# Performance work log

Hardware: AMD Instinct MI355X
Metric: run time of the kernel (lower is better)

Reference implementation:

```python
import jax, jax.numpy as jnp
import numpy as np

MIN_TIMESCALE = 1.0
MAX_TIMESCALE = 10000.0


def llama_rope(x):
    # x: [B, S, N, H]; LLaMA-style interleaved rotary embedding (pairs along last dim).
    B, S, N, H = x.shape
    half = H // 2
    fraction = 2.0 * jnp.arange(0, half, dtype=jnp.float32) / H
    timescale = MIN_TIMESCALE * (MAX_TIMESCALE / MIN_TIMESCALE) ** fraction  # [half]
    position = jnp.arange(S, dtype=jnp.float32)[None, :, None, None]  # [1,S,1,1]
    sinusoid = position / timescale[None, None, None, :]  # [1,S,1,half]
    sin, cos = jnp.sin(sinusoid), jnp.cos(sinusoid)
    xr = x.astype(jnp.float32).reshape(B, S, N, half, 2)
    x1, x2 = xr[..., 0], xr[..., 1]
    r1 = x1 * cos - x2 * sin
    r2 = x2 * cos + x1 * sin
    out = jnp.stack((r1, r2), axis=-1).reshape(B, S, N, H)
    return out.astype(x.dtype)


def setup_inputs() -> dict:
    key = jax.random.key(0)
    kx, kq, kk, kv, ko = jax.random.split(key, 5)
    B, S, D, N, H = 4, 2048, 2048, 16, 128
    x = jax.random.normal(kx, (B, S, D), dtype=jnp.float32)
    # fan_in-style scaling for projection kernels
    wq = jax.random.normal(kq, (D, N, H), dtype=jnp.float32) / np.sqrt(D)
    wk = jax.random.normal(kk, (D, N, H), dtype=jnp.float32) / np.sqrt(D)
    wv = jax.random.normal(kv, (D, N, H), dtype=jnp.float32) / np.sqrt(D)
    wo = jax.random.normal(ko, (N, H, D), dtype=jnp.float32) / np.sqrt(N * H)
    return {"x": x, "wq": wq, "wk": wk, "wv": wv, "wo": wo}


def reference(x, wq, wk, wv, wo):
    # QKV projections (DenseGeneral with features=(num_heads, head_dim))
    q = jnp.einsum("bsd,dnh->bsnh", x, wq)
    k = jnp.einsum("bsd,dnh->bsnh", x, wk)
    v = jnp.einsum("bsd,dnh->bsnh", x, wv)
    # Fused RoPE on query and key (LLaMA interleaved variant)
    q = llama_rope(q)
    k = llama_rope(k)
    head_dim = q.shape[-1]
    q = q / jnp.sqrt(jnp.asarray(head_dim, q.dtype))
    # Causal flash attention (math equivalent: masked softmax attention)
    S = q.shape[1]
    logits = jnp.einsum("bqnh,bknh->bnqk", q, k)  # [B,N,S,S]
    causal = jnp.tril(jnp.ones((S, S), dtype=bool))
    logits = jnp.where(causal[None, None, :, :], logits, jnp.asarray(-1e30, logits.dtype))
    probs = jax.nn.softmax(logits.astype(jnp.float32), axis=-1).astype(v.dtype)
    attn = jnp.einsum("bnqk,bknh->bqnh", probs, v)  # [B,S,N,H]
    # Output projection (DenseGeneral over axes (-2,-1))
    return jnp.einsum("bqnh,nhd->bqd", attn, wo)
```

## Files before the change

kernel.cpp:

```cpp
#include <hip/hip_runtime.h>
#include <hip/hip_bf16.h>
#include <cmath>

#define S_LEN 2048
#define DDIM  2048
#define NHEAD 16
#define HDIM  128
#define BATCH 4
#define KPAD  152
#define VPAD  40
#define PPAD  40

typedef __bf16 bf16;
typedef __attribute__((ext_vector_type(8))) __bf16 bf16x8;
typedef __attribute__((ext_vector_type(4))) __bf16 bf16x4;
typedef __attribute__((ext_vector_type(4))) float  f32x4;

__device__ __forceinline__ void gl_lds(const bf16* g, bf16* l) {
  __builtin_amdgcn_global_load_lds((const __attribute__((address_space(1))) unsigned*)g,
                                   (__attribute__((address_space(3))) unsigned*)l, 16, 0, 0);
}

__global__ __launch_bounds__(256)
void conv_kernel(const float* __restrict__ x, bf16* __restrict__ y) {
  size_t i = ((size_t)blockIdx.x * 256 + threadIdx.x) * 8;
  float4 a = *(const float4*)&x[i];
  float4 b = *(const float4*)&x[i + 4];
  bf16x8 o;
  o[0] = (bf16)a.x; o[1] = (bf16)a.y; o[2] = (bf16)a.z; o[3] = (bf16)a.w;
  o[4] = (bf16)b.x; o[5] = (bf16)b.y; o[6] = (bf16)b.z; o[7] = (bf16)b.w;
  *(bf16x8*)&y[i] = o;
}

__global__ __launch_bounds__(256)
void twconv_kernel(const float* __restrict__ W, bf16* __restrict__ Wt) {
  __shared__ bf16 tile[64][72];
  const int t  = threadIdx.x;
  const int k0 = blockIdx.x * 64;
  const int n0 = blockIdx.y * 64;
#pragma unroll
  for (int it = 0; it < 4; it++) {
    int k = (t >> 4) + it * 16;
    int n = (t & 15) * 4;
    float4 v = *(const float4*)&W[(size_t)(k0 + k) * DDIM + n0 + n];
    tile[k][n + 0] = (bf16)v.x; tile[k][n + 1] = (bf16)v.y;
    tile[k][n + 2] = (bf16)v.z; tile[k][n + 3] = (bf16)v.w;
  }
  __syncthreads();
#pragma unroll
  for (int it = 0; it < 2; it++) {
    int n  = (t >> 3) + it * 32;
    int kc = (t & 7) * 8;
    bf16x8 o;
#pragma unroll
    for (int j = 0; j < 8; j++) o[j] = tile[kc + j][n];
    *(bf16x8*)&Wt[(size_t)(n0 + n) * DDIM + k0 + kc] = o;
  }
}

template <int MODE>
__global__ __launch_bounds__(512, 2)
void gemm_kernel(const bf16* __restrict__ A, const bf16* __restrict__ Bt,
                 void* __restrict__ Out) {
  __shared__ bf16 As[2][256 * 64];
  __shared__ bf16 Bs[2][256 * 64];

  const int t    = threadIdx.x;
  const int m0   = blockIdx.y * 256;
  const int n0   = blockIdx.x * 256;
  const int lane = t & 63;
  const int wave = t >> 6;
  const int wm   = wave >> 2;
  const int wn   = wave & 3;
  const int quad = lane >> 4;
  const int lm   = lane & 15;
  const int sw   = lm & 7;

  const int lrow   = lane >> 3;
  const int lslot  = lane & 7;
  const int lchunk = lslot ^ lrow;

  const int rA = wm * 128 + wn * 32;
  const int rB = (wn >> 1) * 128 + (wm * 2 + (wn & 1)) * 32;
  const bf16* gA = &A [(size_t)(m0 + rA + lrow) * DDIM + lchunk * 8];
  const bf16* gB = &Bt[(size_t)(n0 + rB + lrow) * DDIM + lchunk * 8];

  f32x4 acc[8][4];
#pragma unroll
  for (int i = 0; i < 8; i++)
#pragma unroll
    for (int j = 0; j < 4; j++) acc[i][j] = (f32x4){0.f, 0.f, 0.f, 0.f};

  auto stage = [&](int k0, int b) {
#pragma unroll
    for (int q = 0; q < 4; q++) {
      gl_lds(gA + (size_t)q * 8 * DDIM + k0, &As[b][(rA + q * 8) * 64]);
      gl_lds(gB + (size_t)q * 8 * DDIM + k0, &Bs[b][(rB + q * 8) * 64]);
    }
  };

  stage(0, 0);
  stage(64, 1);
  asm volatile("s_waitcnt vmcnt(8)" ::: "memory");
  __builtin_amdgcn_s_barrier();

  const int NT = DDIM / 64;
#pragma unroll 2
  for (int tt = 0; tt < NT; ++tt) {
    const bf16* as = &As[tt & 1][0];
    const bf16* bs = &Bs[tt & 1][0];
    bf16x8 af[4], bfr[4];

#pragma unroll
    for (int j = 0; j < 4; j++)
      bfr[j] = *(const bf16x8*)&bs[(wn * 64 + j * 16 + lm) * 64 + 8 * (quad ^ sw)];
#pragma unroll
    for (int i = 0; i < 4; i++)
      af[i] = *(const bf16x8*)&as[(wm * 128 + i * 16 + lm) * 64 + 8 * (quad ^ sw)];
    __builtin_amdgcn_s_setprio(1);
#pragma unroll
    for (int i = 0; i < 4; i++)
#pragma unroll
      for (int j = 0; j < 4; j++)
        acc[i][j] = __builtin_amdgcn_mfma_f32_16x16x32_bf16(af[i], bfr[j], acc[i][j], 0, 0, 0);
    __builtin_amdgcn_s_setprio(0);
    __builtin_amdgcn_sched_barrier(0);

#pragma unroll
    for (int i = 0; i < 4; i++)
      af[i] = *(const bf16x8*)&as[(wm * 128 + 64 + i * 16 + lm) * 64 + 8 * (quad ^ sw)];
    __builtin_amdgcn_s_setprio(1);
#pragma unroll
    for (int i = 0; i < 4; i++)
#pragma unroll
      for (int j = 0; j < 4; j++)
        acc[4 + i][j] = __builtin_amdgcn_mfma_f32_16x16x32_bf16(af[i], bfr[j], acc[4 + i][j], 0, 0, 0);
    __builtin_amdgcn_s_setprio(0);
    __builtin_amdgcn_sched_barrier(0);

#pragma unroll
    for (int j = 0; j < 4; j++)
      bfr[j] = *(const bf16x8*)&bs[(wn * 64 + j * 16 + lm) * 64 + 8 * ((4 + quad) ^ sw)];
#pragma unroll
    for (int i = 0; i < 4; i++)
      af[i] = *(const bf16x8*)&as[(wm * 128 + i * 16 + lm) * 64 + 8 * ((4 + quad) ^ sw)];
    __builtin_amdgcn_s_setprio(1);
#pragma unroll
    for (int i = 0; i < 4; i++)
#pragma unroll
      for (int j = 0; j < 4; j++)
        acc[i][j] = __builtin_amdgcn_mfma_f32_16x16x32_bf16(af[i], bfr[j], acc[i][j], 0, 0, 0);
    __builtin_amdgcn_s_setprio(0);
    __builtin_amdgcn_sched_barrier(0);

#pragma unroll
    for (int i = 0; i < 4; i++)
      af[i] = *(const bf16x8*)&as[(wm * 128 + 64 + i * 16 + lm) * 64 + 8 * ((4 + quad) ^ sw)];
    __builtin_amdgcn_s_setprio(1);
#pragma unroll
    for (int i = 0; i < 4; i++)
#pragma unroll
      for (int j = 0; j < 4; j++)
        acc[4 + i][j] = __builtin_amdgcn_mfma_f32_16x16x32_bf16(af[i], bfr[j], acc[4 + i][j], 0, 0, 0);
    __builtin_amdgcn_s_setprio(0);
    __builtin_amdgcn_sched_barrier(0);

    asm volatile("s_waitcnt lgkmcnt(0)" ::: "memory");
    __builtin_amdgcn_s_barrier();
    if (tt + 2 < NT) {
      stage((tt + 2) * 64, tt & 1);
      asm volatile("s_waitcnt vmcnt(8)" ::: "memory");
      __builtin_amdgcn_s_barrier();
    } else if (tt + 1 < NT) {
      asm volatile("s_waitcnt vmcnt(0)" ::: "memory");
      __builtin_amdgcn_s_barrier();
    }
  }

  const int row_base = m0 + wm * 128;
  const int col_base = n0 + wn * 64;

  if constexpr (MODE == 3) {
    float* O = (float*)Out;
#pragma unroll
    for (int m = 0; m < 8; m++)
#pragma unroll
      for (int j = 0; j < 4; j++)
#pragma unroll
        for (int r = 0; r < 4; r++) {
          int row = row_base + (m >> 2) * 64 + (m & 3) * 16 + quad * 4 + r;
          int col = col_base + j * 16 + lm;
          O[(size_t)row * DDIM + col] = acc[m][j][r];
        }
  } else if constexpr (MODE == 2) {
    bf16* O = (bf16*)Out;
#pragma unroll
    for (int m = 0; m < 8; m++) {
      int row = row_base + (m >> 2) * 64 + (m & 3) * 16 + quad * 4;
      int b = row >> 11, s = row & (S_LEN - 1);
#pragma unroll
      for (int j = 0; j < 4; j++) {
        int col = col_base + j * 16 + lm;
        int head = col >> 7, h = col & (HDIM - 1);
        bf16x4 pk;
#pragma unroll
        for (int r = 0; r < 4; r++) pk[r] = (bf16)acc[m][j][r];
        *(bf16x4*)&O[((size_t)(b * NHEAD + head) * HDIM + h) * S_LEN + s] = pk;
      }
    }
  } else {
    bf16* O = (bf16*)Out;
#pragma unroll
    for (int m = 0; m < 8; m++)
#pragma unroll
      for (int j = 0; j < 4; j++)
#pragma unroll
        for (int r = 0; r < 4; r++) {
          int row = row_base + (m >> 2) * 64 + (m & 3) * 16 + quad * 4 + r;
          int col = col_base + j * 16 + lm;
          int b = row >> 11, s = row & (S_LEN - 1);
          int head = col >> 7, h = col & (HDIM - 1);
          float v = acc[m][j][r];
          float partner = __shfl_xor(v, 1, 64);
          float inv_ts = __expf((float)(h >> 1) * -0.14391156831f);
          float ang = (float)s * inv_ts;
          float sn, cs;
          __sincosf(ang, &sn, &cs);
          float o = ((h & 1) == 0) ? (v * cs - partner * sn) : (v * cs + partner * sn);
          if (MODE == 0) o *= 0.08838834764831845f;
          O[((size_t)(b * NHEAD + head) * S_LEN + s) * HDIM + h] = (bf16)o;
        }
  }
}

__global__ __launch_bounds__(256, 2)
void attn_kernel(const bf16* __restrict__ Q, const bf16* __restrict__ K,
                 const bf16* __restrict__ Vt, bf16* __restrict__ Aout) {
  __shared__ bf16 Ks[32 * KPAD];
  __shared__ bf16 Vs[128 * VPAD];
  __shared__ bf16 Pl[4][32 * PPAD];
  const int t    = threadIdx.x;
  const int lane = t & 63;
  const int wave = t >> 6;
  const int quad = lane >> 4;
  const int lm   = lane & 15;
  const int a    = blockIdx.x;
  const int bh   = blockIdx.y;
  const int lobase = a * 64 + wave * 16;
  const int hibase = 2048 - a * 64 - 64 + wave * 16;
  const size_t hb = (size_t)bh * S_LEN * HDIM;
  const bf16* Qh = Q + hb;
  const bf16* Kh = K + hb;
  const bf16* Vh = Vt + hb;
  bf16* P = &Pl[wave][0];

  bf16x8 qflo[4], qfhi[4];
#pragma unroll
  for (int c = 0; c < 4; c++) {
    qflo[c] = *(const bf16x8*)&Qh[(size_t)(lobase + lm) * HDIM + c * 32 + quad * 8];
    qfhi[c] = *(const bf16x8*)&Qh[(size_t)(hibase + lm) * HDIM + c * 32 + quad * 8];
  }

  bf16 onev = (bf16)1.0f;
  bf16x8 ones = {onev, onev, onev, onev, onev, onev, onev, onev};

  f32x4 olo[8], ohi[8];
#pragma unroll
  for (int hc = 0; hc < 8; hc++) {
    olo[hc] = (f32x4){0.f, 0.f, 0.f, 0.f};
    ohi[hc] = (f32x4){0.f, 0.f, 0.f, 0.f};
  }
  f32x4 llo = (f32x4){0.f, 0.f, 0.f, 0.f};
  f32x4 lhi = (f32x4){0.f, 0.f, 0.f, 0.f};

  const int nkt = 64 - 2 * a;
  const int nlo = 2 * a + (wave >> 1) + 1;
  const int nhi = 63 - 2 * a + (wave >> 1);

  const int c0    = t * 2;
  const int krow0 = c0 >> 4, kcol0 = (c0 & 15) * 8;
  const int vrow0 = c0 >> 2, vcol0 = (c0 & 3) * 8;

  for (int kt = 0; kt < nkt; kt++) {
    const int kb = kt * 32;
    __syncthreads();
    {
      const bf16* kg = &Kh[(size_t)(kb + krow0) * HDIM + kcol0];
      *(bf16x8*)&Ks[krow0 * KPAD + kcol0]     = *(const bf16x8*)kg;
      *(bf16x8*)&Ks[krow0 * KPAD + kcol0 + 8] = *(const bf16x8*)(kg + 8);
      const bf16* vg = &Vh[(size_t)vrow0 * S_LEN + kb + vcol0];
      *(bf16x8*)&Vs[vrow0 * VPAD + vcol0]     = *(const bf16x8*)vg;
      *(bf16x8*)&Vs[vrow0 * VPAD + vcol0 + 8] = *(const bf16x8*)(vg + 8);
    }
    __syncthreads();

    const bool hi_act = kt < nhi;
    const bool lo_act = kt < nlo;

    bf16x8 af[2][4];
#pragma unroll
    for (int cb = 0; cb < 2; cb++)
#pragma unroll
      for (int c = 0; c < 4; c++)
        af[cb][c] = *(const bf16x8*)&Ks[(cb * 16 + lm) * KPAD + c * 32 + quad * 8];

    if (hi_act) {
      f32x4 s[2] = {(f32x4){0.f, 0.f, 0.f, 0.f}, (f32x4){0.f, 0.f, 0.f, 0.f}};
#pragma unroll
      for (int c = 0; c < 4; c++)
#pragma unroll
        for (int cb = 0; cb < 2; cb++)
          s[cb] = __builtin_amdgcn_mfma_f32_16x16x32_bf16(af[cb][c], qfhi[c], s[cb], 0, 0, 0);
#pragma unroll
      for (int cb = 0; cb < 2; cb++) {
        bf16x4 pk;
#pragma unroll
        for (int r = 0; r < 4; r++) {
          int key = kb + cb * 16 + quad * 4 + r;
          float sv = (key <= hibase + lm) ? s[cb][r] : -3.0e38f;
          pk[r] = (bf16)__expf(sv - 12.0f);
        }
        *(bf16x4*)&P[(16 + lm) * PPAD + cb * 16 + quad * 4] = pk;
      }
    }
    if (lo_act) {
      f32x4 s[2] = {(f32x4){0.f, 0.f, 0.f, 0.f}, (f32x4){0.f, 0.f, 0.f, 0.f}};
#pragma unroll
      for (int c = 0; c < 4; c++)
#pragma unroll
        for (int cb = 0; cb < 2; cb++)
          s[cb] = __builtin_amdgcn_mfma_f32_16x16x32_bf16(af[cb][c], qflo[c], s[cb], 0, 0, 0);
#pragma unroll
      for (int cb = 0; cb < 2; cb++) {
        bf16x4 pk;
#pragma unroll
        for (int r = 0; r < 4; r++) {
          int key = kb + cb * 16 + quad * 4 + r;
          float sv = (key <= lobase + lm) ? s[cb][r] : -3.0e38f;
          pk[r] = (bf16)__expf(sv - 12.0f);
        }
        *(bf16x4*)&P[lm * PPAD + cb * 16 + quad * 4] = pk;
      }
    }
    __builtin_amdgcn_s_waitcnt(0xC07F);

    bf16x8 vf[8];
#pragma unroll
    for (int hc = 0; hc < 8; hc++)
      vf[hc] = *(const bf16x8*)&Vs[(hc * 16 + lm) * VPAD + quad * 8];

    if (hi_act) {
      bf16x8 pf = *(const bf16x8*)&P[(16 + lm) * PPAD + quad * 8];
#pragma unroll
      for (int hc = 0; hc < 8; hc++)
        ohi[hc] = __builtin_amdgcn_mfma_f32_16x16x32_bf16(pf, vf[hc], ohi[hc], 0, 0, 0);
      lhi = __builtin_amdgcn_mfma_f32_16x16x32_bf16(pf, ones, lhi, 0, 0, 0);
    }
    if (lo_act) {
      bf16x8 pf = *(const bf16x8*)&P[lm * PPAD + quad * 8];
#pragma unroll
      for (int hc = 0; hc < 8; hc++)
        olo[hc] = __builtin_amdgcn_mfma_f32_16x16x32_bf16(pf, vf[hc], olo[hc], 0, 0, 0);
      llo = __builtin_amdgcn_mfma_f32_16x16x32_bf16(pf, ones, llo, 0, 0, 0);
    }
  }

  const int b = bh >> 4, n = bh & 15;
#pragma unroll
  for (int r = 0; r < 4; r++) {
    float invl = 1.0f / llo[r];
    float invh = 1.0f / lhi[r];
    int ql = lobase + quad * 4 + r;
    int qh = hibase + quad * 4 + r;
    size_t bl = ((size_t)(b * S_LEN + ql) * NHEAD + n) * HDIM;
    size_t bhh = ((size_t)(b * S_LEN + qh) * NHEAD + n) * HDIM;
#pragma unroll
    for (int hc = 0; hc < 8; hc++) {
      Aout[bl  + hc * 16 + lm] = (bf16)(olo[hc][r] * invl);
      Aout[bhh + hc * 16 + lm] = (bf16)(ohi[hc][r] * invh);
    }
  }
}

extern "C" void kernel_launch(void* const* d_in, const int* in_sizes, int n_in,
                              void* d_out, int out_size, void* d_ws, size_t ws_size,
                              hipStream_t stream) {
  const float* x  = (const float*)d_in[0];
  const float* wq = (const float*)d_in[1];
  const float* wk = (const float*)d_in[2];
  const float* wv = (const float*)d_in[3];
  const float* wo = (const float*)d_in[4];
  float* out = (float*)d_out;

  const size_t SZ  = (size_t)BATCH * S_LEN * NHEAD * HDIM;
  const size_t WSZ = (size_t)DDIM * DDIM;
  bf16* Qb = (bf16*)d_ws;
  bf16* Kb = Qb + SZ;
  bf16* Vb = Kb + SZ;
  bf16* Eb = Vb + SZ;

  bf16* WTq = (bf16*)d_out;
  bf16* WTk = WTq + WSZ;
  bf16* WTv = WTk + WSZ;
  bf16* WTo = (bf16*)Qb;

  dim3 blk(256);
  conv_kernel<<<SZ / (256 * 8), blk, 0, stream>>>(x, Eb);
  dim3 gt(32, 32);
  twconv_kernel<<<gt, blk, 0, stream>>>(wq, WTq);
  twconv_kernel<<<gt, blk, 0, stream>>>(wk, WTk);
  twconv_kernel<<<gt, blk, 0, stream>>>(wv, WTv);

  dim3 blk2(512);
  dim3 gg(DDIM / 256, (BATCH * S_LEN) / 256);
  gemm_kernel<0><<<gg, blk2, 0, stream>>>(Eb, WTq, (void*)Qb);
  gemm_kernel<1><<<gg, blk2, 0, stream>>>(Eb, WTk, (void*)Kb);
  gemm_kernel<2><<<gg, blk2, 0, stream>>>(Eb, WTv, (void*)Vb);

  dim3 ga(16, BATCH * NHEAD);
  attn_kernel<<<ga, blk, 0, stream>>>(Qb, Kb, Vb, Eb);

  twconv_kernel<<<gt, blk, 0, stream>>>(wo, WTo);
  gemm_kernel<3><<<gg, blk2, 0, stream>>>(Eb, WTo, (void*)out);
}
```

Baseline: 612.5 us.

## Double-buffer K/V tiles in attention and add wave-synchronized phases in GEMM

The attention kernel now keeps two LDS buffers for K and V. It prefetches the tile two steps ahead into registers and writes the next tile to LDS while the current one is computed, so each iteration needs one barrier instead of two. Its launch bounds ask for three blocks per CU instead of two, which tightens the register budget and may cause spills. The projection GEMM loop is no longer unrolled and adds a block barrier plus an LDS wait around each MFMA cluster to keep waves in lockstep, which costs extra synchronization.

Result: slower. 785.3 us (+28.2%).

```diff
diff --git a/kernel.cpp b/kernel.cpp
--- a/kernel.cpp
+++ b/kernel.cpp
@@ -105,11 +105,12 @@
   __builtin_amdgcn_s_barrier();
 
   const int NT = DDIM / 64;
-#pragma unroll 2
+  bf16x8 af[4], bfr[4];
+
+#pragma unroll 1
   for (int tt = 0; tt < NT; ++tt) {
     const bf16* as = &As[tt & 1][0];
     const bf16* bs = &Bs[tt & 1][0];
-    bf16x8 af[4], bfr[4];
 
 #pragma unroll
     for (int j = 0; j < 4; j++)
@@ -117,6 +118,10 @@
 #pragma unroll
     for (int i = 0; i < 4; i++)
       af[i] = *(const bf16x8*)&as[(wm * 128 + i * 16 + lm) * 64 + 8 * (quad ^ sw)];
+    __builtin_amdgcn_sched_barrier(0);
+    __builtin_amdgcn_s_barrier();
+    asm volatile("s_waitcnt lgkmcnt(0)" ::: "memory");
+    __builtin_amdgcn_sched_barrier(0);
     __builtin_amdgcn_s_setprio(1);
 #pragma unroll
     for (int i = 0; i < 4; i++)
@@ -125,10 +130,15 @@
         acc[i][j] = __builtin_amdgcn_mfma_f32_16x16x32_bf16(af[i], bfr[j], acc[i][j], 0, 0, 0);
     __builtin_amdgcn_s_setprio(0);
     __builtin_amdgcn_sched_barrier(0);
+    __builtin_amdgcn_s_barrier();
 
 #pragma unroll
     for (int i = 0; i < 4; i++)
       af[i] = *(const bf16x8*)&as[(wm * 128 + 64 + i * 16 + lm) * 64 + 8 * (quad ^ sw)];
+    __builtin_amdgcn_sched_barrier(0);
+    __builtin_amdgcn_s_barrier();
+    asm volatile("s_waitcnt lgkmcnt(0)" ::: "memory");
+    __builtin_amdgcn_sched_barrier(0);
     __builtin_amdgcn_s_setprio(1);
 #pragma unroll
     for (int i = 0; i < 4; i++)
@@ -137,6 +147,7 @@
         acc[4 + i][j] = __builtin_amdgcn_mfma_f32_16x16x32_bf16(af[i], bfr[j], acc[4 + i][j], 0, 0, 0);
     __builtin_amdgcn_s_setprio(0);
     __builtin_amdgcn_sched_barrier(0);
+    __builtin_amdgcn_s_barrier();
 
 #pragma unroll
     for (int j = 0; j < 4; j++)
@@ -144,6 +155,10 @@
 #pragma unroll
     for (int i = 0; i < 4; i++)
       af[i] = *(const bf16x8*)&as[(wm * 128 + i * 16 + lm) * 64 + 8 * ((4 + quad) ^ sw)];
+    __builtin_amdgcn_sched_barrier(0);
+    __builtin_amdgcn_s_barrier();
+    asm volatile("s_waitcnt lgkmcnt(0)" ::: "memory");
+    __builtin_amdgcn_sched_barrier(0);
     __builtin_amdgcn_s_setprio(1);
 #pragma unroll
     for (int i = 0; i < 4; i++)
@@ -152,10 +167,15 @@
         acc[i][j] = __builtin_amdgcn_mfma_f32_16x16x32_bf16(af[i], bfr[j], acc[i][j], 0, 0, 0);
     __builtin_amdgcn_s_setprio(0);
     __builtin_amdgcn_sched_barrier(0);
+    __builtin_amdgcn_s_barrier();
 
 #pragma unroll
     for (int i = 0; i < 4; i++)
       af[i] = *(const bf16x8*)&as[(wm * 128 + 64 + i * 16 + lm) * 64 + 8 * ((4 + quad) ^ sw)];
+    __builtin_amdgcn_sched_barrier(0);
+    __builtin_amdgcn_s_barrier();
+    asm volatile("s_waitcnt lgkmcnt(0)" ::: "memory");
+    __builtin_amdgcn_sched_barrier(0);
     __builtin_amdgcn_s_setprio(1);
 #pragma unroll
     for (int i = 0; i < 4; i++)
@@ -164,9 +184,8 @@
         acc[4 + i][j] = __builtin_amdgcn_mfma_f32_16x16x32_bf16(af[i], bfr[j], acc[4 + i][j], 0, 0, 0);
     __builtin_amdgcn_s_setprio(0);
     __builtin_amdgcn_sched_barrier(0);
-
-    asm volatile("s_waitcnt lgkmcnt(0)" ::: "memory");
-    __builtin_amdgcn_s_barrier();
+    __builtin_amdgcn_s_barrier();
+
     if (tt + 2 < NT) {
       stage((tt + 2) * 64, tt & 1);
       asm volatile("s_waitcnt vmcnt(8)" ::: "memory");
@@ -233,11 +252,11 @@
   }
 }
 
-__global__ __launch_bounds__(256, 2)
+__global__ __launch_bounds__(256, 3)
 void attn_kernel(const bf16* __restrict__ Q, const bf16* __restrict__ K,
                  const bf16* __restrict__ Vt, bf16* __restrict__ Aout) {
-  __shared__ bf16 Ks[32 * KPAD];
-  __shared__ bf16 Vs[128 * VPAD];
+  __shared__ bf16 Ks[2][32 * KPAD];
+  __shared__ bf16 Vs[2][128 * VPAD];
   __shared__ bf16 Pl[4][32 * PPAD];
   const int t    = threadIdx.x;
   const int lane = t & 63;
@@ -281,18 +300,34 @@
   const int krow0 = c0 >> 4, kcol0 = (c0 & 15) * 8;
   const int vrow0 = c0 >> 2, vcol0 = (c0 & 3) * 8;
 
+  bf16x8 kr0, kr1, vr0, vr1;
+
+  auto ldk = [&](int kt) {
+    const bf16* kg = &Kh[(size_t)(kt * 32 + krow0) * HDIM + kcol0];
+    kr0 = *(const bf16x8*)kg;
+    kr1 = *(const bf16x8*)(kg + 8);
+    const bf16* vg = &Vh[(size_t)vrow0 * S_LEN + kt * 32 + vcol0];
+    vr0 = *(const bf16x8*)vg;
+    vr1 = *(const bf16x8*)(vg + 8);
+  };
+  auto stw = [&](int b) {
+    *(bf16x8*)&Ks[b][krow0 * KPAD + kcol0]     = kr0;
+    *(bf16x8*)&Ks[b][krow0 * KPAD + kcol0 + 8] = kr1;
+    *(bf16x8*)&Vs[b][vrow0 * VPAD + vcol0]     = vr0;
+    *(bf16x8*)&Vs[b][vrow0 * VPAD + vcol0 + 8] = vr1;
+  };
+
+  ldk(0);
+  stw(0);
+  ldk(1);
+  __syncthreads();
+
   for (int kt = 0; kt < nkt; kt++) {
-    const int kb = kt * 32;
-    __syncthreads();
-    {
-      const bf16* kg = &Kh[(size_t)(kb + krow0) * HDIM + kcol0];
-      *(bf16x8*)&Ks[krow0 * KPAD + kcol0]     = *(const bf16x8*)kg;
-      *(bf16x8*)&Ks[krow0 * KPAD + kcol0 + 8] = *(const bf16x8*)(kg + 8);
-      const bf16* vg = &Vh[(size_t)vrow0 * S_LEN + kb + vcol0];
-      *(bf16x8*)&Vs[vrow0 * VPAD + vcol0]     = *(const bf16x8*)vg;
-      *(bf16x8*)&Vs[vrow0 * VPAD + vcol0 + 8] = *(const bf16x8*)(vg + 8);
-    }
-    __syncthreads();
+    const int kb  = kt * 32;
+    const int cur = kt & 1;
+
+    if (kt + 1 < nkt) stw((kt + 1) & 1);
+    if (kt + 2 < nkt) ldk(kt + 2);
 
     const bool hi_act = kt < nhi;
     const bool lo_act = kt < nlo;
@@ -302,7 +337,7 @@
     for (int cb = 0; cb < 2; cb++)
 #pragma unroll
       for (int c = 0; c < 4; c++)
-        af[cb][c] = *(const bf16x8*)&Ks[(cb * 16 + lm) * KPAD + c * 32 + quad * 8];
+        af[cb][c] = *(const bf16x8*)&Ks[cur][(cb * 16 + lm) * KPAD + c * 32 + quad * 8];
 
     if (hi_act) {
       f32x4 s[2] = {(f32x4){0.f, 0.f, 0.f, 0.f}, (f32x4){0.f, 0.f, 0.f, 0.f}};
@@ -347,7 +382,7 @@
     bf16x8 vf[8];
 #pragma unroll
     for (int hc = 0; hc < 8; hc++)
-      vf[hc] = *(const bf16x8*)&Vs[(hc * 16 + lm) * VPAD + quad * 8];
+      vf[hc] = *(const bf16x8*)&Vs[cur][(hc * 16 + lm) * VPAD + quad * 8];
 
     if (hi_act) {
       bf16x8 pf = *(const bf16x8*)&P[(16 + lm) * PPAD + quad * 8];
@@ -363,6 +398,7 @@
         olo[hc] = __builtin_amdgcn_mfma_f32_16x16x32_bf16(pf, vf[hc], olo[hc], 0, 0, 0);
       llo = __builtin_amdgcn_mfma_f32_16x16x32_bf16(pf, ones, llo, 0, 0, 0);
     }
+    __syncthreads();
   }
 
   const int b = bh >> 4, n = bh & 15;
```
